# Kernel tuning notes

Hardware: AMD Instinct MI355X
Metric: run time of the kernel (lower is better)

## Reference

```python
import jax, jax.numpy as jnp
import numpy as np

# Hyperparams matching init_kwargs
KH = KW = KL = 3
SH = SW = SL = 1
PH = PW = PL = 1
DH = DW = DL = 1
DG = 1  # deformable_groups


def _out_dim(s, pad, dil, k, stride):
    return (s + 2 * pad - (dil * (k - 1) + 1)) // stride + 1


def _deform_conv3d(x, offset, mask, weight):
    # x: [N, C, H, W, L]; weight: [Cout, C//groups, KH, KW, KL] (groups=1)
    N, C, H, W, L = x.shape
    Cout = weight.shape[0]
    kprod = KH * KW * KL
    Ho = _out_dim(H, PH, DH, KH, SH)
    Wo = _out_dim(W, PW, DW, KW, SW)
    Lo = _out_dim(L, PL, DL, KL, SL)

    # offset layout: [N, DG, kprod, 3(h,w,l), Ho, Wo, Lo]; mask: [N, DG, kprod, Ho, Wo, Lo]
    off = offset.reshape(N, DG, kprod, 3, Ho, Wo, Lo)
    m = mask.reshape(N, DG, kprod, Ho, Wo, Lo)

    # kernel tap positions (kidx = i*KW*KL + j*KL + k), scaled by dilation
    ki, kj, kk = jnp.meshgrid(jnp.arange(KH), jnp.arange(KW), jnp.arange(KL), indexing='ij')
    kh = (ki.reshape(-1) * DH).astype(jnp.float32)  # [kprod]
    kw = (kj.reshape(-1) * DW).astype(jnp.float32)
    kl = (kk.reshape(-1) * DL).astype(jnp.float32)

    hb = (jnp.arange(Ho) * SH - PH).astype(jnp.float32)
    wb = (jnp.arange(Wo) * SW - PW).astype(jnp.float32)
    lb = (jnp.arange(Lo) * SL - PL).astype(jnp.float32)

    # sampling coordinates: [N, DG, kprod, Ho, Wo, Lo]
    ch = off[:, :, :, 0] + hb[None, None, None, :, None, None] + kh[None, None, :, None, None, None]
    cw = off[:, :, :, 1] + wb[None, None, None, None, :, None] + kw[None, None, :, None, None, None]
    cl = off[:, :, :, 2] + lb[None, None, None, None, None, :] + kl[None, None, :, None, None, None]

    Cpg = C // DG
    xf = x.reshape(N, DG, Cpg, H * W * L)
    P = kprod * Ho * Wo * Lo

    h0 = jnp.floor(ch); w0 = jnp.floor(cw); l0 = jnp.floor(cl)
    fh = ch - h0; fw = cw - w0; fl = cl - l0
    h0i = h0.astype(jnp.int32); w0i = w0.astype(jnp.int32); l0i = l0.astype(jnp.int32)

    # trilinear interpolation: accumulate over 8 corners (zero outside volume)
    val = jnp.zeros((N, DG, Cpg, P), x.dtype)
    for dh in (0, 1):
        for dw in (0, 1):
            for dl in (0, 1):
                ih = h0i + dh; iw = w0i + dw; il = l0i + dl
                wgt = (fh if dh else 1.0 - fh) * (fw if dw else 1.0 - fw) * (fl if dl else 1.0 - fl)
                valid = (ih >= 0) & (ih < H) & (iw >= 0) & (iw < W) & (il >= 0) & (il < L)
                lin = ((jnp.clip(ih, 0, H - 1) * W + jnp.clip(iw, 0, W - 1)) * L
                       + jnp.clip(il, 0, L - 1)).reshape(N, DG, 1, P)
                g = jnp.take_along_axis(xf, jnp.broadcast_to(lin, (N, DG, Cpg, P)), axis=3)
                val = val + g * (wgt * valid).reshape(N, DG, 1, P)

    # modulate by mask, then contract columns with weight (groups=1)
    val = val.reshape(N, DG, Cpg, kprod, Ho, Wo, Lo) * m[:, :, None]
    cols = val.reshape(N, C, kprod, Ho * Wo * Lo)
    out = jnp.einsum('nckp,ock->nop', cols, weight.reshape(Cout, C, kprod))
    return out.reshape(N, Cout, Ho, Wo, Lo)


def setup_inputs() -> dict:
    key = jax.random.key(0)
    k1, k2, k3, k4 = jax.random.split(key, 4)
    N, C, H, W, L = 1, 64, 32, 32, 32
    Cout = 64
    kprod = KH * KW * KL
    Ho = _out_dim(H, PH, DH, KH, SH)
    Wo = _out_dim(W, PW, DW, KW, SW)
    Lo = _out_dim(L, PL, DL, KL, SL)
    x = jax.random.normal(k1, (N, C, H, W, L), jnp.float32)
    offset = jax.random.normal(k2, (N, DG * 3 * kprod, Ho, Wo, Lo), jnp.float32)
    mask = jax.random.uniform(k3, (N, DG * kprod, Ho, Wo, Lo), jnp.float32)
    stdv = 1.0 / np.sqrt(C * kprod)
    weight = jax.random.uniform(k4, (Cout, C, KH, KW, KL), jnp.float32, -stdv, stdv)
    return {"x": x, "offset": offset, "mask": mask, "weight": weight}


def reference(x, offset, mask, weight):
    return _deform_conv3d(x, offset, mask, weight)
```

## Files before the change

kernel.cpp:

```cpp
#include <hip/hip_runtime.h>
#include <hip/hip_bf16.h>

typedef short short8 __attribute__((ext_vector_type(8)));
typedef unsigned int u32x4 __attribute__((ext_vector_type(4)));
typedef float f32x4 __attribute__((ext_vector_type(4)));
typedef float f32x2 __attribute__((ext_vector_type(2)));

#define SPAT  32768
#define KPROD 27

__device__ __constant__ float4 KTAB[KPROD] = {
    {0,0,0,0},{0,0,1,0},{0,0,2,0},{0,1,0,0},{0,1,1,0},{0,1,2,0},{0,2,0,0},{0,2,1,0},{0,2,2,0},
    {1,0,0,0},{1,0,1,0},{1,0,2,0},{1,1,0,0},{1,1,1,0},{1,1,2,0},{1,2,0,0},{1,2,1,0},{1,2,2,0},
    {2,0,0,0},{2,0,1,0},{2,0,2,0},{2,1,0,0},{2,1,1,0},{2,1,2,0},{2,2,0,0},{2,2,1,0},{2,2,2,0}
};

static __device__ __forceinline__ short f2bf(float f) {
    return (short)__bfloat16_as_ushort(__float2bfloat16(f));
}

template<int S>
static __device__ __forceinline__ int qbcast_i(int x) {
    return __builtin_amdgcn_mov_dpp(x, S * 0x55, 0xF, 0xF, true);
}
template<int S>
static __device__ __forceinline__ float qbcast_f(float x) {
    return __int_as_float(qbcast_i<S>(__float_as_int(x)));
}

__global__ void transpose_x_bf16(const float* __restrict__ x, unsigned short* __restrict__ xt) {
    __shared__ float tile[64][65];
    const int t = threadIdx.x;
    const int s0 = blockIdx.x * 64;
    const int lane = t & 63, grp = t >> 6;
#pragma unroll
    for (int r = 0; r < 16; ++r) {
        int c = grp * 16 + r;
        tile[c][lane] = x[c * SPAT + s0 + lane];
    }
    __syncthreads();
#pragma unroll
    for (int r = 0; r < 16; ++r) {
        int srow = grp * 16 + r;
        xt[(s0 + srow) * 64 + lane] = __bfloat16_as_ushort(__float2bfloat16(tile[lane][srow]));
    }
}

__global__ void prep_w_frag(const float* __restrict__ w, unsigned short* __restrict__ wt) {
    int idx = blockIdx.x * 256 + threadIdx.x;
    if (idx >= KPROD * 4096) return;
    int k = idx >> 12;
    int fid = idx & 4095;
    int i = fid >> 9;
    int lane = (fid >> 3) & 63;
    int e = fid & 7;
    int ot = i >> 1, kb = i & 1;
    int o = ot * 16 + (lane & 15);
    int c = kb * 32 + (lane >> 4) * 8 + e;
    wt[idx] = __bfloat16_as_ushort(__float2bfloat16(w[(o * 64 + c) * KPROD + k]));
}

__global__ __launch_bounds__(128)
void dconv3d_ks(const unsigned short* __restrict__ xt, const unsigned short* __restrict__ wf,
                const float* __restrict__ offset, const float* __restrict__ mask,
                float* __restrict__ out0, float* __restrict__ out1, int ngroups) {
    __shared__ float red[16][65];

    const int t    = threadIdx.x;
    const int wid  = t >> 6;
    const int l    = t & 63;
    const int pl   = l & 15;
    const int g    = l >> 4;
    const int gp   = l >> 2;
    const int gg   = l & 3;
    const int dhq  = gg >> 1, dwq = gg & 1;
    const int goff = wid * 64 + gg * 16;
    const int bpidx = (pl * 4 + g) * 4;

    const int grpid = (ngroups == 2) ? (int)blockIdx.y : 0;
    const int k0 = (ngroups == 2) ? grpid * 14 : 0;
    const int nt = (ngroups == 2) ? (14 - grpid) : KPROD;
    float* outp = (grpid == 0) ? out0 : out1;

    const int nwg = (int)gridDim.x;
    const int cpx = nwg >> 3;
    const int bid = (int)blockIdx.x;
    const int bsw = (bid & 7) * cpx + (bid >> 3);

    const int p_base = bsw * 16;
    const int pos_g = p_base + gp;
    const int hog = pos_g >> 10, wog = (pos_g >> 5) & 31, log = pos_g & 31;
    const float fho = (float)(hog - 1), fwo = (float)(wog - 1), flo = (float)(log - 1);
    const char* xbase = (const char*)xt;
    const char* xgg = xbase + goff;

    f32x4 acc[4] = {};

    auto load_off = [&](int k) -> f32x4 {
        f32x4 r;
        r.x = offset[(3 * k + 0) * SPAT + pos_g];
        r.y = offset[(3 * k + 1) * SPAT + pos_g];
        r.z = offset[(3 * k + 2) * SPAT + pos_g];
        r.w = mask[k * SPAT + pos_g];
        return r;
    };

    auto compute_meta = [&](int k, f32x4 om, float w01[2], int o01[2]) {
        float4 kt = KTAB[k];
        float chh = om.x + (fho + kt.x);
        float cww = om.y + (fwo + kt.y);
        float cll = om.z + (flo + kt.z);
        float h0f = floorf(chh), w0f = floorf(cww), l0f = floorf(cll);
        float fh = chh - h0f, fw = cww - w0f, fl = cll - l0f;
        int h0 = (int)h0f, w0 = (int)w0f, l0i = (int)l0f;
        int ih = h0 + dhq, iw = w0 + dwq;
        float wh = dhq ? fh : 1.f - fh;
        float ww = dwq ? fw : 1.f - fw;
        float whwm = wh * ww * om.w;
        float w1v = whwm * fl;
        float w0v = whwm - w1v;
        bool vhw = ((unsigned)ih < 32u) && ((unsigned)iw < 32u);
        bool v0 = vhw && ((unsigned)l0i < 32u);
        bool v1 = vhw && ((unsigned)(l0i + 1) < 32u);
        w01[0] = v0 ? w0v : 0.f;
        w01[1] = v1 ? w1v : 0.f;
        int ihc = min(max(ih, 0), 31), iwc = min(max(iw, 0), 31);
        int l0c = min(max(l0i, 0), 31);
        int l1c = min(max(l0i + 1, 0), 31);
        int base2 = (ihc * 32 + iwc) * 32;
        o01[0] = (base2 + l0c) << 7;
        o01[1] = (base2 + l1c) << 7;
    };

    auto exchange = [&](const float w01[2], const int o01[2], float mwO[8], int moO[8]) {
        mwO[0] = qbcast_f<0>(w01[0]); mwO[1] = qbcast_f<0>(w01[1]);
        mwO[2] = qbcast_f<1>(w01[0]); mwO[3] = qbcast_f<1>(w01[1]);
        mwO[4] = qbcast_f<2>(w01[0]); mwO[5] = qbcast_f<2>(w01[1]);
        mwO[6] = qbcast_f<3>(w01[0]); mwO[7] = qbcast_f<3>(w01[1]);
        moO[0] = qbcast_i<0>(o01[0]); moO[1] = qbcast_i<0>(o01[1]);
        moO[2] = qbcast_i<1>(o01[0]); moO[3] = qbcast_i<1>(o01[1]);
        moO[4] = qbcast_i<2>(o01[0]); moO[5] = qbcast_i<2>(o01[1]);
        moO[6] = qbcast_i<3>(o01[0]); moO[7] = qbcast_i<3>(o01[1]);
    };

    float mw[8];
    u32x4 q[8];
    {
        f32x4 om0 = load_off(k0);
        float w01[2]; int o01[2], mo0[8];
        compute_meta(k0, om0, w01, o01);
        exchange(w01, o01, mw, mo0);
#pragma unroll
        for (int j = 0; j < 8; ++j)
            q[j] = *(const u32x4*)(xgg + mo0[j]);
    }
    f32x4 offA = load_off(k0 + 1);

#pragma unroll 1
    for (int kk = 0; kk < nt; ++kk) {
        const int k = k0 + kk;

        short8 wfr[4];
#pragma unroll
        for (int ot = 0; ot < 4; ++ot)
            wfr[ot] = *(const short8*)&wf[((size_t)k * 8 + ot * 2 + wid) * 512 + l * 8];

        f32x4 offB;
        if (kk + 2 < nt) offB = load_off(k + 2);

        float mwN[8]; int moN[8];
        if (kk + 1 < nt) {
            float w01[2]; int o01[2];
            compute_meta(k + 1, offA, w01, o01);
            exchange(w01, o01, mwN, moN);
        }

        f32x2 v[4] = {};
#pragma unroll
        for (int j = 0; j < 8; ++j) {
            f32x2 w2 = {mw[j], mw[j]};
#pragma unroll
            for (int qd = 0; qd < 4; ++qd) {
                unsigned int a = q[j][qd];
                f32x2 xa = {__uint_as_float(a << 16), __uint_as_float(a & 0xffff0000u)};
                v[qd] = __builtin_elementwise_fma(w2, xa, v[qd]);
            }
        }
        union { short8 s; u32x4 u; } bg;
#pragma unroll
        for (int qd = 0; qd < 4; ++qd) {
            bg.s[2 * qd]     = f2bf(v[qd].x);
            bg.s[2 * qd + 1] = f2bf(v[qd].y);
        }

        if (kk + 1 < nt) {
#pragma unroll
            for (int j = 0; j < 8; ++j)
                q[j] = *(const u32x4*)(xgg + moN[j]);
        }

        union { u32x4 u; short8 s; } bm;
#pragma unroll
        for (int d = 0; d < 4; ++d)
            bm.u[d] = (unsigned)__builtin_amdgcn_ds_bpermute(bpidx, (int)bg.u[d]);

#pragma unroll
        for (int ot = 0; ot < 4; ++ot)
            acc[ot] = __builtin_amdgcn_mfma_f32_16x16x32_bf16(wfr[ot], bm.s, acc[ot], 0, 0, 0);

        if (kk + 1 < nt) {
#pragma unroll
            for (int j = 0; j < 8; ++j) mw[j] = mwN[j];
        }
        offA = offB;
    }

    __syncthreads();
    if (wid == 0) {
#pragma unroll
        for (int ot = 0; ot < 4; ++ot)
#pragma unroll
            for (int r = 0; r < 4; ++r)
                red[pl][ot * 16 + g * 4 + r] = acc[ot][r];
    }
    __syncthreads();
    if (wid == 1) {
#pragma unroll
        for (int ot = 0; ot < 4; ++ot)
#pragma unroll
            for (int r = 0; r < 4; ++r)
                red[pl][ot * 16 + g * 4 + r] += acc[ot][r];
    }
    __syncthreads();

#pragma unroll
    for (int it = 0; it < 8; ++it) {
        int idx = it * 128 + t;
        int p = idx & 15, o = idx >> 4;
        outp[(size_t)o * SPAT + p_base + p] = red[p][o];
    }
}

__global__ void reduce_add(float* __restrict__ out, const float* __restrict__ part) {
    int i = blockIdx.x * 256 + threadIdx.x;
    f32x4 a = ((const f32x4*)out)[i];
    f32x4 b = ((const f32x4*)part)[i];
    a.x += b.x; a.y += b.y; a.z += b.z; a.w += b.w;
    ((f32x4*)out)[i] = a;
}

extern "C" void kernel_launch(void* const* d_in, const int* in_sizes, int n_in,
                              void* d_out, int out_size, void* d_ws, size_t ws_size,
                              hipStream_t stream) {
    const float* x      = (const float*)d_in[0];
    const float* offset = (const float*)d_in[1];
    const float* mask   = (const float*)d_in[2];
    const float* weight = (const float*)d_in[3];
    float* out = (float*)d_out;

    const size_t xt_bytes  = (size_t)SPAT * 64 * 2;
    const size_t wt_bytes  = (size_t)KPROD * 4096 * 2;
    const size_t prt_bytes = (size_t)64 * SPAT * 4;

    unsigned short* xt  = (unsigned short*)d_ws;
    unsigned short* wtb = (unsigned short*)((char*)d_ws + xt_bytes);
    float*          prt = (float*)((char*)d_ws + xt_bytes + wt_bytes);

    const bool split = (ws_size >= xt_bytes + wt_bytes + prt_bytes);
    const int ngroups = split ? 2 : 1;

    hipLaunchKernelGGL(transpose_x_bf16, dim3(SPAT / 64), dim3(256), 0, stream, x, xt);
    hipLaunchKernelGGL(prep_w_frag, dim3((KPROD * 4096 + 255) / 256), dim3(256), 0, stream,
                       weight, wtb);
    hipLaunchKernelGGL(dconv3d_ks, dim3(SPAT / 16, ngroups), dim3(128), 0, stream,
                       xt, wtb, offset, mask, out, prt, ngroups);
    if (split)
        hipLaunchKernelGGL(reduce_add, dim3(64 * SPAT / 4 / 256), dim3(256), 0, stream,
                           out, prt);
}
```

Measured before the change: 82.95 us.

## Move kernel-tap split into the block and reduce partials in shared memory

The two kernel-tap groups previously ran as separate blocks (grid y=2), writing partial outputs to a workspace buffer that a separate reduce_add kernel then summed. Now each block has 4 waves: two waves per tap group, and the two groups' partials are summed in LDS before a single store. This removes the extra 8 MB partial write and read and one kernel launch. In exchange the blocks are larger, and the split is now unconditional rather than gated on workspace size.

Result: slower. 85.50 us (+3.1%).

```diff
diff --git a/kernel.cpp b/kernel.cpp
--- a/kernel.cpp
+++ b/kernel.cpp
@@ -60,14 +60,16 @@
     wt[idx] = __bfloat16_as_ushort(__float2bfloat16(w[(o * 64 + c) * KPROD + k]));
 }
 
-__global__ __launch_bounds__(128)
-void dconv3d_ks(const unsigned short* __restrict__ xt, const unsigned short* __restrict__ wf,
+__global__ __launch_bounds__(256)
+void dconv3d_w4(const unsigned short* __restrict__ xt, const unsigned short* __restrict__ wf,
                 const float* __restrict__ offset, const float* __restrict__ mask,
-                float* __restrict__ out0, float* __restrict__ out1, int ngroups) {
-    __shared__ float red[16][65];
+                float* __restrict__ out) {
+    __shared__ float red[2][16][65];
 
     const int t    = threadIdx.x;
-    const int wid  = t >> 6;
+    const int wid4 = t >> 6;
+    const int wid  = wid4 & 1;
+    const int kgrp = wid4 >> 1;
     const int l    = t & 63;
     const int pl   = l & 15;
     const int g    = l >> 4;
@@ -77,10 +79,8 @@
     const int goff = wid * 64 + gg * 16;
     const int bpidx = (pl * 4 + g) * 4;
 
-    const int grpid = (ngroups == 2) ? (int)blockIdx.y : 0;
-    const int k0 = (ngroups == 2) ? grpid * 14 : 0;
-    const int nt = (ngroups == 2) ? (14 - grpid) : KPROD;
-    float* outp = (grpid == 0) ? out0 : out1;
+    const int k0 = kgrp * 14;
+    const int nt = 14 - kgrp;
 
     const int nwg = (int)gridDim.x;
     const int cpx = nwg >> 3;
@@ -216,37 +216,31 @@
     }
 
     __syncthreads();
-    if (wid == 0) {
+    if (wid4 == 0 || wid4 == 2) {
+        const int tree = wid4 >> 1;
 #pragma unroll
         for (int ot = 0; ot < 4; ++ot)
 #pragma unroll
             for (int r = 0; r < 4; ++r)
-                red[pl][ot * 16 + g * 4 + r] = acc[ot][r];
-    }
-    __syncthreads();
-    if (wid == 1) {
+                red[tree][pl][ot * 16 + g * 4 + r] = acc[ot][r];
+    }
+    __syncthreads();
+    if (wid4 == 1 || wid4 == 3) {
+        const int tree = wid4 >> 1;
 #pragma unroll
         for (int ot = 0; ot < 4; ++ot)
 #pragma unroll
             for (int r = 0; r < 4; ++r)
-                red[pl][ot * 16 + g * 4 + r] += acc[ot][r];
-    }
-    __syncthreads();
-
-#pragma unroll
-    for (int it = 0; it < 8; ++it) {
-        int idx = it * 128 + t;
+                red[tree][pl][ot * 16 + g * 4 + r] += acc[ot][r];
+    }
+    __syncthreads();
+
+#pragma unroll
+    for (int it = 0; it < 4; ++it) {
+        int idx = it * 256 + t;
         int p = idx & 15, o = idx >> 4;
-        outp[(size_t)o * SPAT + p_base + p] = red[p][o];
-    }
-}
-
-__global__ void reduce_add(float* __restrict__ out, const float* __restrict__ part) {
-    int i = blockIdx.x * 256 + threadIdx.x;
-    f32x4 a = ((const f32x4*)out)[i];
-    f32x4 b = ((const f32x4*)part)[i];
-    a.x += b.x; a.y += b.y; a.z += b.z; a.w += b.w;
-    ((f32x4*)out)[i] = a;
+        out[(size_t)o * SPAT + p_base + p] = red[0][p][o] + red[1][p][o];
+    }
 }
 
 extern "C" void kernel_launch(void* const* d_in, const int* in_sizes, int n_in,
@@ -258,23 +252,13 @@
     const float* weight = (const float*)d_in[3];
     float* out = (float*)d_out;
 
-    const size_t xt_bytes  = (size_t)SPAT * 64 * 2;
-    const size_t wt_bytes  = (size_t)KPROD * 4096 * 2;
-    const size_t prt_bytes = (size_t)64 * SPAT * 4;
-
+    const size_t xt_bytes = (size_t)SPAT * 64 * 2;
     unsigned short* xt  = (unsigned short*)d_ws;
     unsigned short* wtb = (unsigned short*)((char*)d_ws + xt_bytes);
-    float*          prt = (float*)((char*)d_ws + xt_bytes + wt_bytes);
-
-    const bool split = (ws_size >= xt_bytes + wt_bytes + prt_bytes);
-    const int ngroups = split ? 2 : 1;
 
     hipLaunchKernelGGL(transpose_x_bf16, dim3(SPAT / 64), dim3(256), 0, stream, x, xt);
     hipLaunchKernelGGL(prep_w_frag, dim3((KPROD * 4096 + 255) / 256), dim3(256), 0, stream,
                        weight, wtb);
-    hipLaunchKernelGGL(dconv3d_ks, dim3(SPAT / 16, ngroups), dim3(128), 0, stream,
-                       xt, wtb, offset, mask, out, prt, ngroups);
-    if (split)
-        hipLaunchKernelGGL(reduce_add, dim3(64 * SPAT / 4 / 256), dim3(256), 0, stream,
-                           out, prt);
-}
+    hipLaunchKernelGGL(dconv3d_w4, dim3(SPAT / 16), dim3(256), 0, stream,
+                       xt, wtb, offset, mask, out);
+}
```
